# Kernel optimization log

Measured on AMD Instinct MI355X. Metric: run time of the kernel, lower is better.

The kernel has to match this reference:

```python
import jax, jax.numpy as jnp
from jax import lax
import numpy as np

N = 20000        # nodes
E = 160000       # directed edges (doubled to 2E inside forward)
NODE_DIM = 6
EDGE_DIM = 4
HID = 64         # hidden_dim
HEADS = 4
ITERS = 3
D_OUT = HEADS * HID          # 256
SQRT_D = 8.0                 # sqrt(HID)
ALLOWED = jnp.array([8., 23., 39., 54., 90., 180.], dtype=jnp.float32)


def _ln(x, g, b):
    m = jnp.mean(x, -1, keepdims=True)
    v = jnp.mean((x - m) ** 2, -1, keepdims=True)
    return (x - m) * lax.rsqrt(v + 1e-5) * g + b


def _cbam(x, w1, b1, w2, b2, cw, cb):
    # channel attention: pool over nodes (dim 0)
    pool = jnp.concatenate([x.max(0, keepdims=True), x.mean(0, keepdims=True)], axis=1)  # [1,2D]
    ch = jax.nn.sigmoid(jnp.maximum(pool @ w1 + b1, 0.) @ w2 + b2)                        # [1,D]
    x = x * ch
    # spatial attention: pool over features, conv1d over node axis
    cat = jnp.concatenate([x.max(-1, keepdims=True), x.mean(-1, keepdims=True)], axis=-1)  # [N,2]
    inp = cat.T[None]                                                                       # [1,2,N]
    sp = lax.conv_general_dilated(inp, cw, (1,), [(3, 3)],
                                  dimension_numbers=('NCH', 'OIH', 'NCH')) + cb[None, :, None]
    return x * jax.nn.sigmoid(sp)[0, 0][:, None]


def _tconv(xc, src, dst, wq, b_q, wk, b_k, wv, b_v, ws, b_s):
    # PyG TransformerConv (concat=True, root_weight=True, no edge features)
    n = xc.shape[0]
    q = (xc @ wq + b_q).reshape(n, HEADS, HID)
    k = (xc @ wk + b_k).reshape(n, HEADS, HID)
    v = (xc @ wv + b_v).reshape(n, HEADS, HID)
    alpha = jnp.einsum('ehd,ehd->eh', q[dst], k[src]) / SQRT_D           # [2E,H]
    amax = jax.ops.segment_max(alpha, dst, num_segments=n)
    a = jnp.exp(alpha - amax[dst])
    a = a / jax.ops.segment_sum(a, dst, num_segments=n)[dst]
    out = jax.ops.segment_sum(a[..., None] * v[src], dst, num_segments=n).reshape(n, D_OUT)
    return out + xc @ ws + b_s


def reference(x, edge_attr, node_w, node_b, edge_w, edge_b, z_emb,
              cn_w1, cn_b1, cn_w2, cn_b2, cn_cw, cn_cb,
              ce_w1, ce_b1, ce_w2, ce_b2, ce_cw, ce_cb,
              Wq, bq, Wk, bk, Wv, bv, Ws, bs,
              lt_g, lt_b, lc_g, lc_b,
              pe_w, pe_b, pn_w, pn_b, gf_w, gf_b,
              c_w1, c_b1, c_w2, c_b2, edge_index):
    send = jnp.concatenate([edge_index[0], edge_index[1]])
    recv = jnp.concatenate([edge_index[1], edge_index[0]])
    src, dst = send, recv                                           # [2E]
    rel = x[src, :3] - x[dst, :3]                                   # [2E,3]
    zi = jnp.argmin(jnp.abs(jnp.round(x[:, 2])[:, None] - ALLOWED[None, :]), axis=1)
    nf = jnp.maximum(x @ node_w + node_b, 0.) + z_emb[zi]           # node embedding + z embedding
    nf = _cbam(nf, cn_w1, cn_b1, cn_w2, cn_b2, cn_cw, cn_cb)
    ef = jnp.concatenate([jnp.concatenate([edge_attr, edge_attr], 0), rel], axis=1)
    ef = jnp.maximum(ef @ edge_w + edge_b, 0.)
    ef = _cbam(ef, ce_w1, ce_b1, ce_w2, ce_b2, ce_cw, ce_cb)
    n = nf.shape[0]
    for i in range(ITERS):
        x0, e0 = nf, ef
        agg = jax.ops.segment_sum(ef, dst, num_segments=n)          # scatter-add messages
        comb = _ln(jnp.concatenate([nf, agg - nf], 1), lc_g[i], lc_b[i])
        out = _tconv(comb, src, dst, Wq[i], bq[i], Wk[i], bk[i], Wv[i], bv[i], Ws[i], bs[i])
        out = _ln(out, lt_g[i], lt_b[i])
        pn = out @ pn_w[i] + pn_b[i]
        g = jax.nn.sigmoid(jnp.concatenate([nf, pn], 1) @ gf_w[i] + gf_b[i])  # gated fusion
        nf = nf * g + pn * (1. - g)
        ef = (out[src] - out[dst]) @ pe_w[i] + pe_b[i]
        nf = nf + x0
        ef = ef + e0
    clf = jnp.concatenate([nf[edge_index[0]], nf[edge_index[1]]], axis=1)
    h = jnp.maximum(clf @ c_w1 + c_b1, 0.)
    return (h @ c_w2 + c_b2)[:, 0]


def setup_inputs() -> dict:
    key = jax.random.key(0)
    ki = iter(jax.random.split(key, 64))
    def rn(shape, s=0.05):
        return jax.random.normal(next(ki), shape, dtype=jnp.float32) * s
    x = jax.random.normal(next(ki), (N, NODE_DIM), dtype=jnp.float32)
    x = x.at[:, 2].set(ALLOWED[jax.random.randint(next(ki), (N,), 0, 6)])
    inp = {
        'x': x,
        'edge_attr': jax.random.normal(next(ki), (E, EDGE_DIM), dtype=jnp.float32),
        'node_w': rn((NODE_DIM, HID)), 'node_b': jnp.zeros(HID),
        'edge_w': rn((EDGE_DIM + 3, HID)), 'edge_b': jnp.zeros(HID),
        'z_emb': rn((6, HID)),
        'cn_w1': rn((2 * HID, HID // 16)), 'cn_b1': jnp.zeros(HID // 16),
        'cn_w2': rn((HID // 16, HID)), 'cn_b2': jnp.zeros(HID),
        'cn_cw': rn((1, 2, 7)), 'cn_cb': jnp.zeros(1),
        'ce_w1': rn((2 * HID, HID // 16)), 'ce_b1': jnp.zeros(HID // 16),
        'ce_w2': rn((HID // 16, HID)), 'ce_b2': jnp.zeros(HID),
        'ce_cw': rn((1, 2, 7)), 'ce_cb': jnp.zeros(1),
        'Wq': rn((ITERS, 2 * HID, D_OUT)), 'bq': jnp.zeros((ITERS, D_OUT)),
        'Wk': rn((ITERS, 2 * HID, D_OUT)), 'bk': jnp.zeros((ITERS, D_OUT)),
        'Wv': rn((ITERS, 2 * HID, D_OUT)), 'bv': jnp.zeros((ITERS, D_OUT)),
        'Ws': rn((ITERS, 2 * HID, D_OUT)), 'bs': jnp.zeros((ITERS, D_OUT)),
        'lt_g': jnp.ones((ITERS, D_OUT)), 'lt_b': jnp.zeros((ITERS, D_OUT)),
        'lc_g': jnp.ones((ITERS, 2 * HID)), 'lc_b': jnp.zeros((ITERS, 2 * HID)),
        'pe_w': rn((ITERS, D_OUT, HID)), 'pe_b': jnp.zeros((ITERS, HID)),
        'pn_w': rn((ITERS, D_OUT, HID)), 'pn_b': jnp.zeros((ITERS, HID)),
        'gf_w': rn((ITERS, 2 * HID, HID)), 'gf_b': jnp.zeros((ITERS, HID)),
        'c_w1': rn((2 * HID, HID)), 'c_b1': jnp.zeros(HID),
        'c_w2': rn((HID, 1)), 'c_b2': jnp.zeros(1),
        'edge_index': jax.random.randint(next(ki), (2, E), 0, N),
    }
    return inp
```

## Files before the change

### kernel.cpp

```cpp
#include <hip/hip_runtime.h>
#include <math.h>

typedef __attribute__((ext_vector_type(8))) short short8;
typedef __attribute__((ext_vector_type(4))) float f32x4;

__device__ __forceinline__ float wave_sum(float v){
  #pragma unroll
  for (int m = 32; m; m >>= 1) v += __shfl_xor(v, m, 64);
  return v;
}
__device__ __forceinline__ float wave_max(float v){
  #pragma unroll
  for (int m = 32; m; m >>= 1) v = fmaxf(v, __shfl_xor(v, m, 64));
  return v;
}
__device__ __forceinline__ unsigned fenc(float f){
  unsigned u = __float_as_uint(f);
  return (u >> 31) ? ~u : (u | 0x80000000u);
}
__device__ __forceinline__ float fdec(unsigned e){
  return (e >> 31) ? __uint_as_float(e & 0x7fffffffu) : __uint_as_float(~e);
}
__device__ __forceinline__ float sigm(float x){ return 1.f / (1.f + __expf(-x)); }
__device__ __forceinline__ unsigned short f2bf(float f){
  union { float f; unsigned u; } x; x.f = f;
  unsigned r = x.u + 0x7fffu + ((x.u >> 16) & 1u);
  return (unsigned short)(r >> 16);
}
__device__ __forceinline__ float bf2f(unsigned short h){
  union { unsigned u; float f; } x; x.u = ((unsigned)h) << 16;
  return x.f;
}

__global__ void k_build_edges(const int* __restrict__ ei, int E2, int E,
                              int* __restrict__ src, int* __restrict__ dst,
                              int* __restrict__ deg){
  int e = blockIdx.x * blockDim.x + threadIdx.x;
  if (e >= E2) return;
  int s = ei[e];
  int d = (e < E) ? ei[e + E] : ei[e - E];
  src[e] = s; dst[e] = d;
  atomicAdd(&deg[d], 1);
}

__global__ void k_scan(const int* __restrict__ deg, int* __restrict__ rowptr, int N){
  __shared__ int part[1024];
  int t = threadIdx.x;
  int chunk = (N + 1023) / 1024;
  int lo = t * chunk, hi = lo + chunk; if (hi > N) hi = N;
  int s = 0;
  for (int i = lo; i < hi; ++i) s += deg[i];
  part[t] = s;
  __syncthreads();
  for (int off = 1; off < 1024; off <<= 1){
    int v = (t >= off) ? part[t - off] : 0;
    __syncthreads();
    part[t] += v;
    __syncthreads();
  }
  int run = part[t] - s;
  for (int i = lo; i < hi; ++i){ rowptr[i] = run; run += deg[i]; }
  if (t == 1023) rowptr[N] = part[1023];
}

__global__ void k_fill(const int* __restrict__ src, const int* __restrict__ dst,
                       const int* __restrict__ rowptr,
                       int* __restrict__ cur, int* __restrict__ csrc,
                       int* __restrict__ epos,
                       const float* __restrict__ x, const float* __restrict__ ea,
                       float* __restrict__ re8, int E2, int E){
  int e = blockIdx.x * blockDim.x + threadIdx.x;
  if (e >= E2) return;
  int s = src[e], d = dst[e];
  int pos = rowptr[d] + atomicAdd(&cur[d], 1);
  csrc[pos] = s;
  epos[e] = pos;
  int row = (e < E) ? e : e - E;
  float4 eav = *reinterpret_cast<const float4*>(ea + (size_t)row*4);
  float r0 = x[s*6]     - x[d*6];
  float r1 = x[s*6 + 1] - x[d*6 + 1];
  float r2 = x[s*6 + 2] - x[d*6 + 2];
  *reinterpret_cast<float4*>(re8 + (size_t)e*8)     = eav;
  *reinterpret_cast<float4*>(re8 + (size_t)e*8 + 4) = make_float4(r0, r1, r2, 0.f);
}

__global__ void k_embed_pool(const float* __restrict__ x, const float* __restrict__ nw,
                             const float* __restrict__ nb, const float* __restrict__ zemb,
                             float* __restrict__ nf,
                             unsigned* __restrict__ pmax, float* __restrict__ psum, int N){
  int tx = threadIdx.x & 63;
  int ty = threadIdx.x >> 6;
  const float allowed[6] = {8.f, 23.f, 39.f, 54.f, 90.f, 180.f};
  float m = -INFINITY, s = 0.f;
  for (int n = blockIdx.x*4 + ty; n < N; n += gridDim.x*4){
    float xv[6];
    #pragma unroll
    for (int k = 0; k < 6; ++k) xv[k] = x[n*6 + k];
    float v = nb[tx];
    #pragma unroll
    for (int k = 0; k < 6; ++k) v += xv[k] * nw[k*64 + tx];
    v = fmaxf(v, 0.f);
    float r = rintf(xv[2]);
    int zi = 0; float bd = fabsf(r - allowed[0]);
    #pragma unroll
    for (int k = 1; k < 6; ++k){ float d = fabsf(r - allowed[k]); if (d < bd){ bd = d; zi = k; } }
    v += zemb[zi*64 + tx];
    nf[(size_t)n*64 + tx] = v;
    m = fmaxf(m, v); s += v;
  }
  __shared__ float sm[4][64], ss[4][64];
  sm[ty][tx] = m; ss[ty][tx] = s;
  __syncthreads();
  if (ty == 0){
    #pragma unroll
    for (int k = 1; k < 4; ++k){ m = fmaxf(m, sm[k][tx]); s += ss[k][tx]; }
    atomicMax(&pmax[tx], fenc(m));
    atomicAdd(&psum[tx], s);
  }
}

__global__ void k_cbam_mlp(const unsigned* __restrict__ pmax, const float* __restrict__ psum,
                           float invR,
                           const float* __restrict__ w1, const float* __restrict__ b1,
                           const float* __restrict__ w2, const float* __restrict__ b2,
                           float* __restrict__ ch){
  __shared__ float pool[128];
  __shared__ float h[4];
  int t = threadIdx.x;
  pool[t]      = fdec(pmax[t]);
  pool[64 + t] = psum[t] * invR;
  __syncthreads();
  if (t < 4){
    float a = b1[t];
    for (int k = 0; k < 128; ++k) a += pool[k] * w1[k*4 + t];
    h[t] = fmaxf(a, 0.f);
  }
  __syncthreads();
  float a = b2[t];
  #pragma unroll
  for (int k = 0; k < 4; ++k) a += h[k] * w2[k*64 + t];
  ch[t] = sigm(a);
}

__global__ void k_chmul_rowpool(float* __restrict__ buf, const float* __restrict__ ch,
                                float* __restrict__ rp, int R){
  int r = blockIdx.x*4 + (threadIdx.x >> 6);
  if (r >= R) return;
  int l = threadIdx.x & 63;
  float v = buf[(size_t)r*64 + l] * ch[l];
  buf[(size_t)r*64 + l] = v;
  float m = wave_max(v);
  float s = wave_sum(v);
  if (l == 0){ rp[(size_t)r*2] = m; rp[(size_t)r*2 + 1] = s * (1.f/64.f); }
}

__global__ void k_spatial(float* __restrict__ buf, const float* __restrict__ rp,
                          const float* __restrict__ cw, const float* __restrict__ cb,
                          unsigned short* __restrict__ gin, int R){
  int r = blockIdx.x*4 + (threadIdx.x >> 6);
  if (r >= R) return;
  int l = threadIdx.x & 63;
  float sp = cb[0];
  #pragma unroll
  for (int t = 0; t < 7; ++t){
    int rr = r + t - 3;
    if (rr >= 0 && rr < R)
      sp += cw[t] * rp[(size_t)rr*2] + cw[7 + t] * rp[(size_t)rr*2 + 1];
  }
  float v = buf[(size_t)r*64 + l] * sigm(sp);
  buf[(size_t)r*64 + l] = v;
  gin[(size_t)r*128 + l] = f2bf(v);
}

__global__ __launch_bounds__(256) void k_ecol(
    const float* __restrict__ re8,
    const float* __restrict__ ew, const float* __restrict__ eb,
    unsigned* __restrict__ pmax, float* __restrict__ psum, int E2){
  __shared__ float s_re[2][1024];
  int tid = threadIdx.x;
  int tx = tid & 63, wv = tid >> 6;
  float ewr[7];
  #pragma unroll
  for (int k = 0; k < 7; ++k) ewr[k] = ew[k*64 + tx];
  float ebl = eb[tx];
  const int CHUNK = 128;
  int base0  = blockIdx.x * CHUNK;
  int stride = gridDim.x * CHUNK;
  float m = -INFINITY, s = 0.f;
  if (base0 < E2){
    int g0 = base0 * 8;
    #pragma unroll
    for (int q = 0; q < 4; ++q){
      int idx = q*256 + tid;
      int gi = g0 + idx;
      s_re[0][idx] = (gi < E2*8) ? re8[gi] : 0.f;
    }
  }
  int buf = 0;
  for (int base = base0; base < E2; base += stride){
    __syncthreads();
    int nb = base + stride;
    if (nb < E2){
      int g0 = nb * 8;
      #pragma unroll
      for (int q = 0; q < 4; ++q){
        int idx = q*256 + tid;
        int gi = g0 + idx;
        s_re[buf ^ 1][idx] = (gi < E2*8) ? re8[gi] : 0.f;
      }
    }
    const float* sb = s_re[buf];
    #pragma unroll
    for (int j = 0; j < 32; ++j){
      int e = base + wv*32 + j;
      if (e < E2){
        const float* r = &sb[(wv*32 + j)*8];
        float v = ebl;
        #pragma unroll
        for (int k = 0; k < 7; ++k) v += r[k] * ewr[k];
        v = fmaxf(v, 0.f);
        m = fmaxf(m, v); s += v;
      }
    }
    buf ^= 1;
  }
  __shared__ float sm[4][64], ss[4][64];
  sm[wv][tx] = m; ss[wv][tx] = s;
  __syncthreads();
  if (wv == 0){
    #pragma unroll
    for (int k = 1; k < 4; ++k){ m = fmaxf(m, sm[k][tx]); s += ss[k][tx]; }
    atomicMax(&pmax[tx], fenc(m));
    atomicAdd(&psum[tx], s);
  }
}

__global__ __launch_bounds__(256) void k_erp2(
    const float* __restrict__ re8, const int* __restrict__ epos,
    const float* __restrict__ ew, const float* __restrict__ eb,
    const float* __restrict__ ch,
    float* __restrict__ rp, float* __restrict__ ef0, int E2){
  __shared__ float s_re[256];
  __shared__ int   s_ep[32];
  int tid = threadIdx.x;
  int tx = tid & 63, wv = tid >> 6;
  float ewr[7];
  #pragma unroll
  for (int k = 0; k < 7; ++k) ewr[k] = ew[k*64 + tx];
  float ebl = eb[tx], chl = ch[tx];
  for (int base = blockIdx.x*32; base < E2; base += gridDim.x*32){
    __syncthreads();
    int gidx = base*8 + tid;
    s_re[tid] = (gidx < E2*8) ? re8[gidx] : 0.f;
    if (tid < 32 && base + tid < E2) s_ep[tid] = epos[base + tid];
    __syncthreads();
    #pragma unroll
    for (int j = 0; j < 8; ++j){
      int e = base + wv*8 + j;
      if (e >= E2) break;
      const float* r = &s_re[(wv*8 + j)*8];
      float v = ebl;
      #pragma unroll
      for (int k = 0; k < 7; ++k) v += r[k] * ewr[k];
      v = fmaxf(v, 0.f) * chl;
      float mm = wave_max(v);
      float sm2 = wave_sum(v);
      if (tx == 0){ rp[(size_t)e*2] = mm; rp[(size_t)e*2 + 1] = sm2 * (1.f/64.f); }
      ef0[(size_t)s_ep[wv*8 + j]*64 + tx] = v;
    }
  }
}

__global__ void k_se(const float* __restrict__ rp, const int* __restrict__ epos,
                     const float* __restrict__ ccw, const float* __restrict__ ccb,
                     float* __restrict__ se, int E2){
  int e = blockIdx.x * blockDim.x + threadIdx.x;
  if (e >= E2) return;
  float sp = ccb[0];
  #pragma unroll
  for (int t = 0; t < 7; ++t){
    int rr = e + t - 3;
    if (rr >= 0 && rr < E2)
      sp += ccw[t] * rp[(size_t)rr*2] + ccw[7+t] * rp[(size_t)rr*2 + 1];
  }
  se[epos[e]] = sigm(sp);
}

__global__ void k_aggb(const float* __restrict__ ef0, const float* __restrict__ se,
                       const int* __restrict__ rowptr, const float* __restrict__ nf,
                       const float* __restrict__ g, const float* __restrict__ b,
                       float* __restrict__ agg, unsigned short* __restrict__ comb, int N){
  int n = blockIdx.x*4 + (threadIdx.x >> 6);
  if (n >= N) return;
  int l = threadIdx.x & 63;
  int lo = rowptr[n], hi = rowptr[n+1];
  float acc = 0.f;
  int i = lo;
  for (; i + 4 <= hi; i += 4){
    float s0 = se[i], s1 = se[i+1], s2 = se[i+2], s3 = se[i+3];
    float e0 = ef0[(size_t)i*64 + l];
    float e1 = ef0[(size_t)(i+1)*64 + l];
    float e2 = ef0[(size_t)(i+2)*64 + l];
    float e3 = ef0[(size_t)(i+3)*64 + l];
    acc += s0*e0 + s1*e1 + s2*e2 + s3*e3;
  }
  for (; i < hi; ++i) acc += se[i] * ef0[(size_t)i*64 + l];
  agg[(size_t)n*64 + l] = acc;
  float a = nf[(size_t)n*64 + l];
  float v0 = a, v1 = acc - a;
  float mean = wave_sum(v0 + v1) * (1.f/128.f);
  float d0 = v0 - mean, d1 = v1 - mean;
  float var = wave_sum(d0*d0 + d1*d1) * (1.f/128.f);
  float rs = rsqrtf(var + 1e-5f);
  comb[(size_t)n*128 + l]      = f2bf(d0 * rs * g[l]      + b[l]);
  comb[(size_t)n*128 + 64 + l] = f2bf(d1 * rs * g[64 + l] + b[64 + l]);
}

__global__ __launch_bounds__(256) void k_packT1(
    const float* __restrict__ Wq, const float* __restrict__ Wk,
    const float* __restrict__ Wv, const float* __restrict__ Ws,
    unsigned short* __restrict__ Bt){
  __shared__ float t[64][65];
  int bx = blockIdx.x, by = blockIdx.y, bz = blockIdx.z;
  const float* W = (bz == 0) ? Wq : (bz == 1) ? Wk : (bz == 2) ? Wv : Ws;
  int tx = threadIdx.x & 63, ty = threadIdx.x >> 6;
  int R0 = by*64, C0 = bx*64;
  for (int r = ty; r < 64; r += 4)
    t[r][tx] = W[(size_t)(R0 + r)*256 + C0 + tx];
  __syncthreads();
  int iter = by >> 1, kr0 = (by & 1)*64;
  for (int r = ty; r < 64; r += 4)
    Bt[(size_t)iter*1024*128 + (size_t)(bz*256 + C0 + r)*128 + kr0 + tx] = f2bf(t[tx][r]);
}

__global__ __launch_bounds__(256) void k_packT2(
    const float* __restrict__ Wn, const float* __restrict__ We,
    unsigned short* __restrict__ Bt2){
  __shared__ float t[64][65];
  int by = blockIdx.y, bz = blockIdx.z;
  const float* W = (bz == 0) ? Wn : We;
  int tx = threadIdx.x & 63, ty = threadIdx.x >> 6;
  int R0 = by*64;
  for (int r = ty; r < 64; r += 4)
    t[r][tx] = W[(size_t)(R0 + r)*64 + tx];
  __syncthreads();
  int iter = by >> 2, kr0 = (by & 3)*64;
  for (int r = ty; r < 64; r += 4)
    Bt2[(size_t)iter*128*256 + (size_t)(bz*64 + r)*256 + kr0 + tx] = f2bf(t[tx][r]);
}

__global__ void k_packG(const float* __restrict__ gfw, unsigned short* __restrict__ BtG){
  int b = blockIdx.x;
  int iter = b >> 7, col = b & 127;
  int k = threadIdx.x;
  unsigned short v = 0;
  if (col < 64) v = f2bf(gfw[(size_t)iter*128*64 + (size_t)k*64 + col]);
  BtG[(size_t)b*128 + k] = v;
}

__global__ void k_biasp(const float* __restrict__ bq, const float* __restrict__ bk,
                        const float* __restrict__ bv, const float* __restrict__ bs,
                        const float* __restrict__ pnb, const float* __restrict__ gfb,
                        float* __restrict__ bias, float* __restrict__ bias2,
                        float* __restrict__ bias3){
  int i = blockIdx.x, t = threadIdx.x;
  const float* bb = (t < 256) ? bq : (t < 512) ? bk : (t < 768) ? bv : bs;
  bias[i*1024 + t] = bb[i*256 + (t & 255)];
  if (t < 64){
    bias2[i*128 + t] = pnb[i*64 + t];
    bias3[i*128 + t] = gfb[i*64 + t];
  } else if (t < 128){
    bias2[i*128 + t] = 0.f;
    bias3[i*128 + t] = 0.f;
  }
}

__global__ void k_packC(const float* __restrict__ cw1, float* __restrict__ Wp){
  int idx = blockIdx.x * blockDim.x + threadIdx.x;
  if (idx >= 64*128) return;
  int k = idx >> 7, j = idx & 127;
  Wp[idx] = (j < 64) ? cw1[k*64 + j] : cw1[(64 + k)*64 + (j - 64)];
}

template<int NSTEPS, int MODE>
__global__ __launch_bounds__(256) void k_mfma(
    const unsigned short* __restrict__ A, int lda,
    const unsigned short* __restrict__ Bt, int ldb,
    const float* __restrict__ bias,
    float* __restrict__ o_f0, unsigned short* __restrict__ o_h0,
    unsigned short* __restrict__ o_h1, float* __restrict__ o_f1, int M){
  __shared__ char lds[65536];
  char* ldsA = lds;
  char* ldsB = lds + 32768;
  int tid = threadIdx.x;
  int nbase = blockIdx.x * 128;
  int mbase = blockIdx.y * 128;
  int l = tid & 63, wid = tid >> 6;
  int wm = (wid >> 1) * 64, wn = (wid & 1) * 64;
  f32x4 acc[4][4] = {};
  const char* Ab  = (const char*)A;
  const char* Btb = (const char*)Bt;
  for (int ks = 0; ks < NSTEPS; ++ks){
    #pragma unroll
    for (int it = 0; it < 8; ++it){
      int c = tid + it*256;
      int row = c >> 4;
      int kb = (c & 15) << 4;
      int off = (row << 8) + (kb ^ ((row & 7) << 4));
      uint4 va = make_uint4(0,0,0,0);
      int gr = mbase + row;
      if (gr < M)
        va = *reinterpret_cast<const uint4*>(Ab + (size_t)gr*(lda*2) + ks*256 + kb);
      *reinterpret_cast<uint4*>(ldsA + off) = va;
      uint4 vb = *reinterpret_cast<const uint4*>(
                   Btb + (size_t)(nbase + row)*(ldb*2) + ks*256 + kb);
      *reinterpret_cast<uint4*>(ldsB + off) = vb;
    }
    __syncthreads();
    #pragma unroll
    for (int kk = 0; kk < 4; ++kk){
      int kbyte = kk*64 + (l >> 4)*16;
      short8 af[4], bf[4];
      #pragma unroll
      for (int m = 0; m < 4; ++m){
        int fr = wm + m*16 + (l & 15);
        af[m] = *reinterpret_cast<const short8*>(ldsA + (fr << 8) + (kbyte ^ ((fr & 7) << 4)));
      }
      #pragma unroll
      for (int n = 0; n < 4; ++n){
        int fc = wn + n*16 + (l & 15);
        bf[n] = *reinterpret_cast<const short8*>(ldsB + (fc << 8) + (kbyte ^ ((fc & 7) << 4)));
      }
      #pragma unroll
      for (int m = 0; m < 4; ++m)
        #pragma unroll
        for (int n = 0; n < 4; ++n)
          acc[m][n] = __builtin_amdgcn_mfma_f32_16x16x32_bf16(af[m], bf[n], acc[m][n], 0, 0, 0);
    }
    __syncthreads();
  }
  #pragma unroll
  for (int n = 0; n < 4; ++n){
    int gcol = nbase + wn + n*16 + (l & 15);
    float bv = bias ? bias[gcol] : 0.f;
    #pragma unroll
    for (int m = 0; m < 4; ++m){
      int grow = mbase + wm + m*16 + (l >> 4)*4;
      #pragma unroll
      for (int r = 0; r < 4; ++r){
        int gr = grow + r;
        if (gr < M){
          float val = acc[m][n][r] + bv;
          if (MODE == 1){
            o_f0[(size_t)gr*128 + gcol] = val;
            if (gcol < 64) o_h0[(size_t)gr*128 + 64 + gcol] = f2bf(val);
          } else if (MODE == 2){
            if (gcol < 64) o_f0[(size_t)gr*64 + gcol] = val;
          } else {
            int seg = gcol >> 8, c = gcol & 255;
            if      (seg == 0) o_f0[(size_t)gr*256 + c] = val;
            else if (seg == 1) o_h0[(size_t)gr*256 + c] = f2bf(val);
            else if (seg == 2) o_h1[(size_t)gr*256 + c] = f2bf(val);
            else               o_f1[(size_t)gr*256 + c] = val;
          }
        }
      }
    }
  }
}

__global__ void k_attn(const float* __restrict__ q, const unsigned short* __restrict__ kbuf,
                       const unsigned short* __restrict__ vbuf, const float* __restrict__ sbuf,
                       const int* __restrict__ rowptr, const int* __restrict__ csrc,
                       const float* __restrict__ ltg, const float* __restrict__ ltb,
                       unsigned short* __restrict__ outb, int N){
  int n = blockIdx.x*4 + (threadIdx.x >> 6);
  if (n >= N) return;
  int l = threadIdx.x & 63;
  int lo = rowptr[n], hi = rowptr[n+1];
  size_t base = (size_t)n*256 + l*4;
  const int l4 = l*4;
  float4 qv = *reinterpret_cast<const float4*>(q + base);
  qv.x *= 0.125f; qv.y *= 0.125f; qv.z *= 0.125f; qv.w *= 0.125f;
  float o0 = 0.f, o1 = 0.f, o2 = 0.f, o3 = 0.f, s = 0.f;
  int i = lo;
  for (; i + 8 <= hi; i += 8){
    ushort4 kk[8], vv[8];
    #pragma unroll
    for (int j = 0; j < 8; ++j){
      int c = csrc[i + j];
      kk[j] = *reinterpret_cast<const ushort4*>(kbuf + (size_t)c*256 + l4);
      vv[j] = *reinterpret_cast<const ushort4*>(vbuf + (size_t)c*256 + l4);
    }
    float a[8];
    #pragma unroll
    for (int j = 0; j < 8; ++j)
      a[j] = qv.x*bf2f(kk[j].x) + qv.y*bf2f(kk[j].y) + qv.z*bf2f(kk[j].z) + qv.w*bf2f(kk[j].w);
    #pragma unroll
    for (int m = 1; m < 16; m <<= 1){
      #pragma unroll
      for (int j = 0; j < 8; ++j) a[j] += __shfl_xor(a[j], m, 64);
    }
    #pragma unroll
    for (int j = 0; j < 8; ++j){
      float w = __expf(a[j]);
      s += w;
      o0 += w*bf2f(vv[j].x); o1 += w*bf2f(vv[j].y);
      o2 += w*bf2f(vv[j].z); o3 += w*bf2f(vv[j].w);
    }
  }
  for (; i < hi; ++i){
    size_t sb = (size_t)csrc[i]*256 + l4;
    ushort4 kv = *reinterpret_cast<const ushort4*>(kbuf + sb);
    ushort4 vv = *reinterpret_cast<const ushort4*>(vbuf + sb);
    float a = qv.x*bf2f(kv.x) + qv.y*bf2f(kv.y) + qv.z*bf2f(kv.z) + qv.w*bf2f(kv.w);
    #pragma unroll
    for (int m = 1; m < 16; m <<= 1) a += __shfl_xor(a, m, 64);
    float w = __expf(a);
    s += w;
    o0 += w*bf2f(vv.x); o1 += w*bf2f(vv.y); o2 += w*bf2f(vv.z); o3 += w*bf2f(vv.w);
  }
  float4 t = *reinterpret_cast<const float4*>(sbuf + base);
  if (hi > lo){
    float r = 1.f / s;
    t.x += o0*r; t.y += o1*r; t.z += o2*r; t.w += o3*r;
  }
  float mean = wave_sum(t.x + t.y + t.z + t.w) * (1.f/256.f);
  float dx = t.x - mean, dy = t.y - mean, dz = t.z - mean, dw = t.w - mean;
  float var = wave_sum(dx*dx + dy*dy + dz*dz + dw*dw) * (1.f/256.f);
  float rs = rsqrtf(var + 1e-5f);
  float4 g = *reinterpret_cast<const float4*>(ltg + l4);
  float4 b = *reinterpret_cast<const float4*>(ltb + l4);
  ushort4 o;
  o.x = f2bf(dx*rs*g.x + b.x);
  o.y = f2bf(dy*rs*g.y + b.y);
  o.z = f2bf(dz*rs*g.z + b.z);
  o.w = f2bf(dw*rs*g.w + b.w);
  *reinterpret_cast<ushort4*>(outb + base) = o;
}

__global__ __launch_bounds__(256) void k_gate2(
    float* __restrict__ nf, float* __restrict__ agg,
    const float* __restrict__ pnP, const float* __restrict__ gate_arg,
    const int* __restrict__ rowptr, const int* __restrict__ csrc,
    const float* __restrict__ peb,
    const float* __restrict__ cg, const float* __restrict__ cbv,
    unsigned short* __restrict__ comb, unsigned short* __restrict__ gin,
    int doComb, int N){
  int n = blockIdx.x*4 + (threadIdx.x >> 6);
  if (n >= N) return;
  int l = threadIdx.x & 63;
  float g = sigm(gate_arg[(size_t)n*64 + l]);
  float nfv = nf[(size_t)n*64 + l];
  float pnv = pnP[(size_t)n*128 + l];
  float nfn = nfv * (1.f + g) + pnv * (1.f - g);
  nf[(size_t)n*64 + l] = nfn;
  gin[(size_t)n*128 + l] = f2bf(nfn);
  int lo = rowptr[n], hi = rowptr[n+1];
  float sp = 0.f;
  int i = lo;
  for (; i + 8 <= hi; i += 8){
    float pv[8];
    #pragma unroll
    for (int j = 0; j < 8; ++j)
      pv[j] = pnP[(size_t)csrc[i+j]*128 + 64 + l];
    #pragma unroll
    for (int j = 0; j < 8; ++j) sp += pv[j];
  }
  for (; i < hi; ++i) sp += pnP[(size_t)csrc[i]*128 + 64 + l];
  float Pn = pnP[(size_t)n*128 + 64 + l];
  float aggn = agg[(size_t)n*64 + l] + sp - (float)(hi - lo) * (Pn - peb[l]);
  agg[(size_t)n*64 + l] = aggn;
  if (doComb){
    float v0 = nfn, v1 = aggn - nfn;
    float mean = wave_sum(v0 + v1) * (1.f/128.f);
    float d0 = v0 - mean, d1 = v1 - mean;
    float var = wave_sum(d0*d0 + d1*d1) * (1.f/128.f);
    float rs = rsqrtf(var + 1e-5f);
    comb[(size_t)n*128 + l]      = f2bf(d0 * rs * cg[l]      + cbv[l]);
    comb[(size_t)n*128 + 64 + l] = f2bf(d1 * rs * cg[64 + l] + cbv[64 + l]);
  }
}

template<int K, int BN>
__global__ __launch_bounds__(256) void k_gemm(
    const float* __restrict__ in, const float* __restrict__ W, int ldw,
    const float* __restrict__ bias, float* __restrict__ out, int ldo, int nrows){
  constexpr int PAD = BN + 4;
  __shared__ float s_in[K * PAD];
  int n0 = blockIdx.x * BN;
  int tid = threadIdx.x;
  for (int idx = tid; idx < BN * K; idx += 256){
    int r = idx / K, k = idx - r * K;
    float v = (n0 + r < nrows) ? in[(size_t)(n0 + r) * K + k] : 0.f;
    s_in[k * PAD + r] = v;
  }
  __syncthreads();
  int tx = tid & 15, ty = tid >> 4;
  constexpr int NT = BN / 16;
  int col0 = blockIdx.y * 64 + tx * 4;
  float acc[NT][4] = {};
  for (int k = 0; k < K; ++k){
    const float4 wv = *reinterpret_cast<const float4*>(&W[(size_t)k * ldw + col0]);
    #pragma unroll
    for (int i = 0; i < NT; ++i){
      float cv = s_in[k * PAD + ty * NT + i];
      acc[i][0] += cv * wv.x;
      acc[i][1] += cv * wv.y;
      acc[i][2] += cv * wv.z;
      acc[i][3] += cv * wv.w;
    }
  }
  #pragma unroll
  for (int i = 0; i < NT; ++i){
    int n = n0 + ty * NT + i;
    if (n < nrows){
      float4 o = make_float4(acc[i][0], acc[i][1], acc[i][2], acc[i][3]);
      *reinterpret_cast<float4*>(&out[(size_t)n * ldo + col0]) = o;
    }
  }
}

__global__ void k_final(const float* __restrict__ AB,
                        const int* __restrict__ ei, const float* __restrict__ cb1,
                        const float* __restrict__ cw2, const float* __restrict__ cb2,
                        float* __restrict__ dout, int E){
  int e = blockIdx.x*4 + (threadIdx.x >> 6);
  if (e >= E) return;
  int l = threadIdx.x & 63;
  int i0 = ei[e], i1 = ei[E + e];
  float h = fmaxf(AB[(size_t)i0*128 + l] + AB[(size_t)i1*128 + 64 + l] + cb1[l], 0.f);
  float p = wave_sum(h * cw2[l]);
  if (l == 0) dout[e] = p + cb2[0];
}

extern "C" void kernel_launch(void* const* d_in, const int* in_sizes, int n_in,
                              void* d_out, int out_size, void* d_ws, size_t ws_size,
                              hipStream_t stream){
  const float* x         = (const float*)d_in[0];
  const float* edge_attr = (const float*)d_in[1];
  const float* node_w    = (const float*)d_in[2];
  const float* node_b    = (const float*)d_in[3];
  const float* edge_w    = (const float*)d_in[4];
  const float* edge_b    = (const float*)d_in[5];
  const float* z_emb     = (const float*)d_in[6];
  const float* cn_w1     = (const float*)d_in[7];
  const float* cn_b1     = (const float*)d_in[8];
  const float* cn_w2     = (const float*)d_in[9];
  const float* cn_b2     = (const float*)d_in[10];
  const float* cn_cw     = (const float*)d_in[11];
  const float* cn_cb     = (const float*)d_in[12];
  const float* ce_w1     = (const float*)d_in[13];
  const float* ce_b1     = (const float*)d_in[14];
  const float* ce_w2     = (const float*)d_in[15];
  const float* ce_b2     = (const float*)d_in[16];
  const float* ce_cw     = (const float*)d_in[17];
  const float* ce_cb     = (const float*)d_in[18];
  const float* Wq        = (const float*)d_in[19];
  const float* bq        = (const float*)d_in[20];
  const float* Wk        = (const float*)d_in[21];
  const float* bk        = (const float*)d_in[22];
  const float* Wv        = (const float*)d_in[23];
  const float* bv        = (const float*)d_in[24];
  const float* Ws        = (const float*)d_in[25];
  const float* bs        = (const float*)d_in[26];
  const float* lt_g      = (const float*)d_in[27];
  const float* lt_b      = (const float*)d_in[28];
  const float* lc_g      = (const float*)d_in[29];
  const float* lc_b      = (const float*)d_in[30];
  const float* pe_w      = (const float*)d_in[31];
  const float* pe_b      = (const float*)d_in[32];
  const float* pn_w      = (const float*)d_in[33];
  const float* pn_b      = (const float*)d_in[34];
  const float* gf_w      = (const float*)d_in[35];
  const float* gf_b      = (const float*)d_in[36];
  const float* c_w1      = (const float*)d_in[37];
  const float* c_b1      = (const float*)d_in[38];
  const float* c_w2      = (const float*)d_in[39];
  const float* c_b2      = (const float*)d_in[40];
  const int*   edge_index= (const int*)d_in[41];

  const int N  = in_sizes[0] / 6;
  const int E  = in_sizes[1] / 4;
  const int E2 = 2 * E;

  char* p = (char*)d_ws;
  auto alloc = [&](size_t bytes)->char*{
    char* r = p; p += (bytes + 255) & ~(size_t)255; return r;
  };
  char* zbase = p;
  int*            w_deg    = (int*)           alloc((size_t)N * 4);
  int*            w_cur    = (int*)           alloc((size_t)N * 4);
  unsigned*       w_pmax   = (unsigned*)      alloc(64 * 4);
  float*          w_psum   = (float*)         alloc(64 * 4);
  unsigned*       w_pmax2  = (unsigned*)      alloc(64 * 4);
  float*          w_psum2  = (float*)         alloc(64 * 4);
  size_t zbytes = (size_t)(p - zbase);
  int*            w_src    = (int*)           alloc((size_t)E2 * 4);
  int*            w_dst    = (int*)           alloc((size_t)E2 * 4);
  int*            w_rowptr = (int*)           alloc((size_t)(N + 1) * 4);
  int*            w_csrc   = (int*)           alloc((size_t)E2 * 4);
  int*            w_epos   = (int*)           alloc((size_t)E2 * 4);
  float*          w_re8    = (float*)         alloc((size_t)E2 * 8 * 4);
  float*          w_nf     = (float*)         alloc((size_t)N * 64 * 4);
  float*          w_agg    = (float*)         alloc((size_t)N * 64 * 4);
  float*          w_ef0    = (float*)         alloc((size_t)E2 * 64 * 4);
  float*          w_se     = (float*)         alloc((size_t)E2 * 4);
  unsigned short* w_comb   = (unsigned short*)alloc((size_t)N * 128 * 2);
  unsigned short* w_gin    = (unsigned short*)alloc((size_t)N * 128 * 2);
  float*          w_gate   = (float*)         alloc((size_t)N * 64 * 4);
  float*          w_q      = (float*)         alloc((size_t)N * 256 * 4);
  unsigned short* w_k      = (unsigned short*)alloc((size_t)N * 256 * 2);
  unsigned short* w_v      = (unsigned short*)alloc((size_t)N * 256 * 2);
  float*          w_s      = (float*)         alloc((size_t)N * 256 * 4);
  unsigned short* w_outb   = (unsigned short*)alloc((size_t)N * 256 * 2);
  float*          w_pnP    = (float*)         alloc((size_t)N * 128 * 4);
  float*          w_rp     = (float*)         alloc((size_t)E2 * 2 * 4);
  float*          w_AB     = (float*)         alloc((size_t)N * 128 * 4);
  float*          w_Wp     = (float*)         alloc((size_t)64 * 128 * 4);
  unsigned short* w_Bt     = (unsigned short*)alloc((size_t)3 * 1024 * 128 * 2);
  float*          w_bias   = (float*)         alloc((size_t)3 * 1024 * 4);
  unsigned short* w_Bt2    = (unsigned short*)alloc((size_t)3 * 128 * 256 * 2);
  float*          w_bias2  = (float*)         alloc((size_t)3 * 128 * 4);
  unsigned short* w_BtG    = (unsigned short*)alloc((size_t)3 * 128 * 128 * 2);
  float*          w_bias3  = (float*)         alloc((size_t)3 * 128 * 4);
  float*          w_ch     = (float*)         alloc(64 * 4);
  float*          w_ch2    = (float*)         alloc(64 * 4);

  hipMemsetAsync(zbase, 0, zbytes, stream);

  k_build_edges<<<(E2 + 255)/256, 256, 0, stream>>>(edge_index, E2, E, w_src, w_dst, w_deg);
  k_scan<<<1, 1024, 0, stream>>>(w_deg, w_rowptr, N);
  k_fill<<<(E2 + 255)/256, 256, 0, stream>>>(w_src, w_dst, w_rowptr, w_cur, w_csrc, w_epos,
                                             x, edge_attr, w_re8, E2, E);
  k_embed_pool<<<256, 256, 0, stream>>>(x, node_w, node_b, z_emb, w_nf, w_pmax, w_psum, N);
  k_cbam_mlp<<<1, 64, 0, stream>>>(w_pmax, w_psum, 1.f/(float)N,
                                   cn_w1, cn_b1, cn_w2, cn_b2, w_ch);
  k_chmul_rowpool<<<(N + 3)/4, 256, 0, stream>>>(w_nf, w_ch, w_rp, N);
  k_spatial<<<(N + 3)/4, 256, 0, stream>>>(w_nf, w_rp, cn_cw, cn_cb, w_gin, N);

  k_ecol<<<256, 256, 0, stream>>>(w_re8, edge_w, edge_b, w_pmax2, w_psum2, E2);
  k_cbam_mlp<<<1, 64, 0, stream>>>(w_pmax2, w_psum2, 1.f/(float)E2,
                                   ce_w1, ce_b1, ce_w2, ce_b2, w_ch2);
  k_erp2<<<2048, 256, 0, stream>>>(w_re8, w_epos, edge_w, edge_b, w_ch2,
                                   w_rp, w_ef0, E2);
  k_se<<<(E2 + 255)/256, 256, 0, stream>>>(w_rp, w_epos, ce_cw, ce_cb, w_se, E2);
  k_aggb<<<(N + 3)/4, 256, 0, stream>>>(w_ef0, w_se, w_rowptr, w_nf,
                                        lc_g, lc_b, w_agg, w_comb, N);

  k_packT1<<<dim3(4, 6, 4), 256, 0, stream>>>(Wq, Wk, Wv, Ws, w_Bt);
  k_packT2<<<dim3(1, 12, 2), 256, 0, stream>>>(pn_w, pe_w, w_Bt2);
  k_packG<<<3*128, 128, 0, stream>>>(gf_w, w_BtG);
  k_biasp<<<3, 1024, 0, stream>>>(bq, bk, bv, bs, pn_b, gf_b, w_bias, w_bias2, w_bias3);
  k_packC<<<32, 256, 0, stream>>>(c_w1, w_Wp);

  const int MB = (N + 127) / 128;
  for (int i = 0; i < 3; ++i){
    k_mfma<1,0><<<dim3(8, MB), 256, 0, stream>>>(w_comb, 128,
                                                 w_Bt + (size_t)i*1024*128, 128,
                                                 w_bias + (size_t)i*1024,
                                                 w_q, w_k, w_v, w_s, N);
    k_attn<<<(N + 3)/4, 256, 0, stream>>>(w_q, w_k, w_v, w_s, w_rowptr, w_csrc,
                                          lt_g + (size_t)i*256, lt_b + (size_t)i*256,
                                          w_outb, N);
    k_mfma<2,1><<<dim3(1, MB), 256, 0, stream>>>(w_outb, 256,
                                                 w_Bt2 + (size_t)i*128*256, 256,
                                                 w_bias2 + (size_t)i*128,
                                                 w_pnP, w_gin, nullptr, nullptr, N);
    k_mfma<1,2><<<dim3(1, MB), 256, 0, stream>>>(w_gin, 128,
                                                 w_BtG + (size_t)i*128*128, 128,
                                                 w_bias3 + (size_t)i*128,
                                                 w_gate, nullptr, nullptr, nullptr, N);
    int doComb = (i < 2) ? 1 : 0;
    const float* cg  = lc_g + (size_t)(i < 2 ? i+1 : 0)*128;
    const float* cbv = lc_b + (size_t)(i < 2 ? i+1 : 0)*128;
    k_gate2<<<(N + 3)/4, 256, 0, stream>>>(w_nf, w_agg, w_pnP, w_gate,
                                           w_rowptr, w_csrc,
                                           pe_b + (size_t)i*64,
                                           cg, cbv, w_comb, w_gin, doComb, N);
  }

  dim3 gAB((N + 63)/64, 2);
  k_gemm<64,64><<<gAB, 256, 0, stream>>>(w_nf, w_Wp, 128, nullptr, w_AB, 128, N);
  k_final<<<(E + 3)/4, 256, 0, stream>>>(w_AB, edge_index, c_b1, c_w2, c_b2,
                                         (float*)d_out, E);
}
```

Baseline: 753.9 us.

## Store edge features in bf16, interleave K/V rows, double-buffer edge staging

Edge features ef0 are now written and read as bf16 instead of fp32, halving the scattered write traffic in k_erp2 and the gather traffic in k_aggb. K and V are packed into a single interleaved [N,512] buffer, so each attention gather reads K and V from the same row. k_erp2 processes 128-edge chunks with double-buffered shared-memory prefetch on half the grid, and k_aggb unrolls its gather by 8. bf16 storage of the edge features adds rounding error to the aggregated edge messages.

```diff
diff --git a/kernel.cpp b/kernel.cpp
--- a/kernel.cpp
+++ b/kernel.cpp
@@ -239,35 +239,60 @@
     const float* __restrict__ re8, const int* __restrict__ epos,
     const float* __restrict__ ew, const float* __restrict__ eb,
     const float* __restrict__ ch,
-    float* __restrict__ rp, float* __restrict__ ef0, int E2){
-  __shared__ float s_re[256];
-  __shared__ int   s_ep[32];
+    float* __restrict__ rp, unsigned short* __restrict__ ef0, int E2){
+  __shared__ float s_re[2][1024];
+  __shared__ int   s_ep[2][128];
   int tid = threadIdx.x;
   int tx = tid & 63, wv = tid >> 6;
   float ewr[7];
   #pragma unroll
   for (int k = 0; k < 7; ++k) ewr[k] = ew[k*64 + tx];
   float ebl = eb[tx], chl = ch[tx];
-  for (int base = blockIdx.x*32; base < E2; base += gridDim.x*32){
+  const int CHUNK = 128;
+  int base0  = blockIdx.x * CHUNK;
+  int stride = gridDim.x * CHUNK;
+  if (base0 < E2){
+    int g0 = base0 * 8;
+    #pragma unroll
+    for (int q = 0; q < 4; ++q){
+      int idx = q*256 + tid;
+      int gi = g0 + idx;
+      s_re[0][idx] = (gi < E2*8) ? re8[gi] : 0.f;
+    }
+    if (tid < 128 && base0 + tid < E2) s_ep[0][tid] = epos[base0 + tid];
+  }
+  int buf = 0;
+  for (int base = base0; base < E2; base += stride){
     __syncthreads();
-    int gidx = base*8 + tid;
-    s_re[tid] = (gidx < E2*8) ? re8[gidx] : 0.f;
-    if (tid < 32 && base + tid < E2) s_ep[tid] = epos[base + tid];
-    __syncthreads();
-    #pragma unroll
-    for (int j = 0; j < 8; ++j){
-      int e = base + wv*8 + j;
-      if (e >= E2) break;
-      const float* r = &s_re[(wv*8 + j)*8];
-      float v = ebl;
+    int nb = base + stride;
+    if (nb < E2){
+      int g0 = nb * 8;
       #pragma unroll
-      for (int k = 0; k < 7; ++k) v += r[k] * ewr[k];
-      v = fmaxf(v, 0.f) * chl;
-      float mm = wave_max(v);
-      float sm2 = wave_sum(v);
-      if (tx == 0){ rp[(size_t)e*2] = mm; rp[(size_t)e*2 + 1] = sm2 * (1.f/64.f); }
-      ef0[(size_t)s_ep[wv*8 + j]*64 + tx] = v;
-    }
+      for (int q = 0; q < 4; ++q){
+        int idx = q*256 + tid;
+        int gi = g0 + idx;
+        s_re[buf ^ 1][idx] = (gi < E2*8) ? re8[gi] : 0.f;
+      }
+      if (tid < 128 && nb + tid < E2) s_ep[buf ^ 1][tid] = epos[nb + tid];
+    }
+    const float* sb = s_re[buf];
+    const int* sep = s_ep[buf];
+    #pragma unroll
+    for (int j = 0; j < 32; ++j){
+      int e = base + wv*32 + j;
+      if (e < E2){
+        const float* r = &sb[(wv*32 + j)*8];
+        float v = ebl;
+        #pragma unroll
+        for (int k = 0; k < 7; ++k) v += r[k] * ewr[k];
+        v = fmaxf(v, 0.f) * chl;
+        float mm = wave_max(v);
+        float sm2 = wave_sum(v);
+        if (tx == 0){ rp[(size_t)e*2] = mm; rp[(size_t)e*2 + 1] = sm2 * (1.f/64.f); }
+        ef0[(size_t)sep[wv*32 + j]*64 + tx] = f2bf(v);
+      }
+    }
+    buf ^= 1;
   }
 }
 
@@ -286,7 +311,7 @@
   se[epos[e]] = sigm(sp);
 }
 
-__global__ void k_aggb(const float* __restrict__ ef0, const float* __restrict__ se,
+__global__ void k_aggb(const unsigned short* __restrict__ ef0, const float* __restrict__ se,
                        const int* __restrict__ rowptr, const float* __restrict__ nf,
                        const float* __restrict__ g, const float* __restrict__ b,
                        float* __restrict__ agg, unsigned short* __restrict__ comb, int N){
@@ -296,15 +321,16 @@
   int lo = rowptr[n], hi = rowptr[n+1];
   float acc = 0.f;
   int i = lo;
-  for (; i + 4 <= hi; i += 4){
-    float s0 = se[i], s1 = se[i+1], s2 = se[i+2], s3 = se[i+3];
-    float e0 = ef0[(size_t)i*64 + l];
-    float e1 = ef0[(size_t)(i+1)*64 + l];
-    float e2 = ef0[(size_t)(i+2)*64 + l];
-    float e3 = ef0[(size_t)(i+3)*64 + l];
-    acc += s0*e0 + s1*e1 + s2*e2 + s3*e3;
-  }
-  for (; i < hi; ++i) acc += se[i] * ef0[(size_t)i*64 + l];
+  for (; i + 8 <= hi; i += 8){
+    float sv[8], ev[8];
+    #pragma unroll
+    for (int j = 0; j < 8; ++j) sv[j] = se[i + j];
+    #pragma unroll
+    for (int j = 0; j < 8; ++j) ev[j] = bf2f(ef0[(size_t)(i + j)*64 + l]);
+    #pragma unroll
+    for (int j = 0; j < 8; ++j) acc += sv[j] * ev[j];
+  }
+  for (; i < hi; ++i) acc += se[i] * bf2f(ef0[(size_t)i*64 + l]);
   agg[(size_t)n*64 + l] = acc;
   float a = nf[(size_t)n*64 + l];
   float v0 = a, v1 = acc - a;
@@ -388,7 +414,7 @@
     const unsigned short* __restrict__ Bt, int ldb,
     const float* __restrict__ bias,
     float* __restrict__ o_f0, unsigned short* __restrict__ o_h0,
-    unsigned short* __restrict__ o_h1, float* __restrict__ o_f1, int M){
+    float* __restrict__ o_f1, int M){
   __shared__ char lds[65536];
   char* ldsA = lds;
   char* ldsB = lds + 32768;
@@ -459,8 +485,8 @@
           } else {
             int seg = gcol >> 8, c = gcol & 255;
             if      (seg == 0) o_f0[(size_t)gr*256 + c] = val;
-            else if (seg == 1) o_h0[(size_t)gr*256 + c] = f2bf(val);
-            else if (seg == 2) o_h1[(size_t)gr*256 + c] = f2bf(val);
+            else if (seg == 1) o_h0[(size_t)gr*512 + c] = f2bf(val);
+            else if (seg == 2) o_h0[(size_t)gr*512 + 256 + c] = f2bf(val);
             else               o_f1[(size_t)gr*256 + c] = val;
           }
         }
@@ -469,8 +495,8 @@
   }
 }
 
-__global__ void k_attn(const float* __restrict__ q, const unsigned short* __restrict__ kbuf,
-                       const unsigned short* __restrict__ vbuf, const float* __restrict__ sbuf,
+__global__ void k_attn(const float* __restrict__ q, const unsigned short* __restrict__ kv,
+                       const float* __restrict__ sbuf,
                        const int* __restrict__ rowptr, const int* __restrict__ csrc,
                        const float* __restrict__ ltg, const float* __restrict__ ltb,
                        unsigned short* __restrict__ outb, int N){
@@ -488,9 +514,9 @@
     ushort4 kk[8], vv[8];
     #pragma unroll
     for (int j = 0; j < 8; ++j){
-      int c = csrc[i + j];
-      kk[j] = *reinterpret_cast<const ushort4*>(kbuf + (size_t)c*256 + l4);
-      vv[j] = *reinterpret_cast<const ushort4*>(vbuf + (size_t)c*256 + l4);
+      const unsigned short* row = kv + (size_t)csrc[i + j]*512 + l4;
+      kk[j] = *reinterpret_cast<const ushort4*>(row);
+      vv[j] = *reinterpret_cast<const ushort4*>(row + 256);
     }
     float a[8];
     #pragma unroll
@@ -510,10 +536,10 @@
     }
   }
   for (; i < hi; ++i){
-    size_t sb = (size_t)csrc[i]*256 + l4;
-    ushort4 kv = *reinterpret_cast<const ushort4*>(kbuf + sb);
-    ushort4 vv = *reinterpret_cast<const ushort4*>(vbuf + sb);
-    float a = qv.x*bf2f(kv.x) + qv.y*bf2f(kv.y) + qv.z*bf2f(kv.z) + qv.w*bf2f(kv.w);
+    const unsigned short* row = kv + (size_t)csrc[i]*512 + l4;
+    ushort4 kk = *reinterpret_cast<const ushort4*>(row);
+    ushort4 vv = *reinterpret_cast<const ushort4*>(row + 256);
+    float a = qv.x*bf2f(kk.x) + qv.y*bf2f(kk.y) + qv.z*bf2f(kk.z) + qv.w*bf2f(kk.w);
     #pragma unroll
     for (int m = 1; m < 16; m <<= 1) a += __shfl_xor(a, m, 64);
     float w = __expf(a);
@@ -704,14 +730,13 @@
   float*          w_re8    = (float*)         alloc((size_t)E2 * 8 * 4);
   float*          w_nf     = (float*)         alloc((size_t)N * 64 * 4);
   float*          w_agg    = (float*)         alloc((size_t)N * 64 * 4);
-  float*          w_ef0    = (float*)         alloc((size_t)E2 * 64 * 4);
+  unsigned short* w_ef0    = (unsigned short*)alloc((size_t)E2 * 64 * 2);
   float*          w_se     = (float*)         alloc((size_t)E2 * 4);
   unsigned short* w_comb   = (unsigned short*)alloc((size_t)N * 128 * 2);
   unsigned short* w_gin    = (unsigned short*)alloc((size_t)N * 128 * 2);
   float*          w_gate   = (float*)         alloc((size_t)N * 64 * 4);
   float*          w_q      = (float*)         alloc((size_t)N * 256 * 4);
-  unsigned short* w_k      = (unsigned short*)alloc((size_t)N * 256 * 2);
-  unsigned short* w_v      = (unsigned short*)alloc((size_t)N * 256 * 2);
+  unsigned short* w_kv     = (unsigned short*)alloc((size_t)N * 512 * 2);
   float*          w_s      = (float*)         alloc((size_t)N * 256 * 4);
   unsigned short* w_outb   = (unsigned short*)alloc((size_t)N * 256 * 2);
   float*          w_pnP    = (float*)         alloc((size_t)N * 128 * 4);
@@ -742,7 +767,7 @@
   k_ecol<<<256, 256, 0, stream>>>(w_re8, edge_w, edge_b, w_pmax2, w_psum2, E2);
   k_cbam_mlp<<<1, 64, 0, stream>>>(w_pmax2, w_psum2, 1.f/(float)E2,
                                    ce_w1, ce_b1, ce_w2, ce_b2, w_ch2);
-  k_erp2<<<2048, 256, 0, stream>>>(w_re8, w_epos, edge_w, edge_b, w_ch2,
+  k_erp2<<<1024, 256, 0, stream>>>(w_re8, w_epos, edge_w, edge_b, w_ch2,
                                    w_rp, w_ef0, E2);
   k_se<<<(E2 + 255)/256, 256, 0, stream>>>(w_rp, w_epos, ce_cw, ce_cb, w_se, E2);
   k_aggb<<<(N + 3)/4, 256, 0, stream>>>(w_ef0, w_se, w_rowptr, w_nf,
@@ -759,18 +784,18 @@
     k_mfma<1,0><<<dim3(8, MB), 256, 0, stream>>>(w_comb, 128,
                                                  w_Bt + (size_t)i*1024*128, 128,
                                                  w_bias + (size_t)i*1024,
-                                                 w_q, w_k, w_v, w_s, N);
-    k_attn<<<(N + 3)/4, 256, 0, stream>>>(w_q, w_k, w_v, w_s, w_rowptr, w_csrc,
+                                                 w_q, w_kv, w_s, N);
+    k_attn<<<(N + 3)/4, 256, 0, stream>>>(w_q, w_kv, w_s, w_rowptr, w_csrc,
                                           lt_g + (size_t)i*256, lt_b + (size_t)i*256,
                                           w_outb, N);
     k_mfma<2,1><<<dim3(1, MB), 256, 0, stream>>>(w_outb, 256,
                                                  w_Bt2 + (size_t)i*128*256, 256,
                                                  w_bias2 + (size_t)i*128,
-                                                 w_pnP, w_gin, nullptr, nullptr, N);
+                                                 w_pnP, w_gin, nullptr, N);
     k_mfma<1,2><<<dim3(1, MB), 256, 0, stream>>>(w_gin, 128,
                                                  w_BtG + (size_t)i*128*128, 128,
                                                  w_bias3 + (size_t)i*128,
-                                                 w_gate, nullptr, nullptr, nullptr, N);
+                                                 w_gate, nullptr, nullptr, N);
     int doComb = (i < 2) ? 1 : 0;
     const float* cg  = lc_g + (size_t)(i < 2 ? i+1 : 0)*128;
     const float* cbv = lc_b + (size_t)(i < 2 ? i+1 : 0)*128;
```

Measured after the change: 745.9 us. Within noise of the previous version (-1.1%).
